# Kernel optimization log

Measured on AMD Instinct MI355X. Metric: run time of the kernel, lower is better.

## Reference

```python
import jax, jax.numpy as jnp
import numpy as np

B, S, E, H = 2, 2048, 1024, 16
D = E // H


def setup_inputs() -> dict:
    key = jax.random.key(0)
    ks = jax.random.split(key, 8)
    hidden_states = jax.random.normal(ks[0], (B, S, E), dtype=jnp.float32)
    # q/k/v projections: small random init
    Wq = jax.random.normal(ks[1], (E, E), dtype=jnp.float32) * 0.02
    Wk = jax.random.normal(ks[2], (E, E), dtype=jnp.float32) * 0.02
    Wv = jax.random.normal(ks[3], (E, E), dtype=jnp.float32) * 0.02
    bq = jnp.zeros((E,), jnp.float32)
    bk = jnp.zeros((E,), jnp.float32)
    bv = jnp.zeros((E,), jnp.float32)
    # hedgehog feature maps: identity init (per init_weights_) + small noise
    eye = jnp.eye(E, dtype=jnp.float32)
    Wfq = eye + jax.random.normal(ks[4], (E, E), dtype=jnp.float32) * 0.02
    Wfk = eye + jax.random.normal(ks[5], (E, E), dtype=jnp.float32) * 0.02
    bfq = jnp.zeros((E,), jnp.float32)
    bfk = jnp.zeros((E,), jnp.float32)
    return dict(hidden_states=hidden_states, Wq=Wq, bq=bq, Wk=Wk, bk=bk,
                Wv=Wv, bv=bv, Wfq=Wfq, bfq=bfq, Wfk=Wfk, bfk=bfk)


def reference(hidden_states, Wq, bq, Wk, bk, Wv, bv, Wfq, bfq, Wfk, bfk):
    b, s, e = hidden_states.shape
    d = e // H
    # feature maps: linear -> linear -> softmax over full hidden dim (before head split)
    q = jax.nn.softmax((hidden_states @ Wq.T + bq) @ Wfq.T + bfq, axis=-1)
    k = jax.nn.softmax((hidden_states @ Wk.T + bk) @ Wfk.T + bfk, axis=-1)
    v = hidden_states @ Wv.T + bv
    split = lambda t: t.reshape(b, s, H, d).transpose(0, 2, 1, 3)  # [B,H,S,D]
    q, k, v = split(q), split(k), split(v)
    scores = jnp.einsum('bhsd,bhtd->bhst', q, k)          # [B,H,S,S], nonnegative
    probs = scores / jnp.sum(scores, axis=-1, keepdims=True)  # sum-normalization
    ctx = jnp.einsum('bhst,bhtd->bhsd', probs, v)
    return ctx.transpose(0, 2, 1, 3).reshape(b, s, e)
```

## Files before the change

kernel.cpp:

```cpp
#include <hip/hip_runtime.h>
#include <math.h>

constexpr int B = 2, S = 2048, E = 1024, H = 16, D = 64;
constexpr int M = B * S;
constexpr int NBIG = 3072;
constexpr int CH = 8;

typedef __attribute__((ext_vector_type(8))) _Float16 half8;
typedef __attribute__((ext_vector_type(4))) float f32x4;
#define MFMA_F16 __builtin_amdgcn_mfma_f32_16x16x32_f16
#define WAITCNT_VM(N) __builtin_amdgcn_s_waitcnt(0xF70 | (N))

__device__ __forceinline__ short f2h(float f) {
  _Float16 h = (_Float16)f;
  short s;
  __builtin_memcpy(&s, &h, 2);
  return s;
}
__device__ __forceinline__ float h2f(short s) {
  _Float16 h;
  __builtin_memcpy(&h, &s, 2);
  return (float)h;
}

__device__ __forceinline__ void gload16(const void* g, const void* l) {
  __builtin_amdgcn_global_load_lds(
      (const __attribute__((address_space(1))) unsigned*)g,
      (__attribute__((address_space(3))) unsigned*)l, 16, 0, 0);
}

template <int BM>
__device__ __forceinline__ void gemm_core(const short* __restrict__ A,
                                          const short* __restrict__ Bm,
                                          int bm, int bn, int K, short* lds,
                                          f32x4 (&acc)[BM / 32][4]) {
  constexpr int SA = BM / 16, TOT = SA + 8, PW = TOT / 4, MT = BM / 32;
  const int tid = threadIdx.x, wave = tid >> 6, lane = tid & 63;

  const short* gb[PW];
#pragma unroll
  for (int j = 0; j < PW; ++j) {
    const int n = wave * PW + j;
    const short* src; int seg, rowbase;
    if (n < SA) { src = A;  seg = n;      rowbase = bm; }
    else        { src = Bm; seg = n - SA; rowbase = bn; }
    const int r = seg * 16 + (lane >> 2);
    const int p = lane & 3;
    const int q = (p - ((r >> 1) & 3)) & 3;
    gb[j] = src + (size_t)(rowbase + r) * K + q * 8;
  }
  const int fr = lane & 15, fq = lane >> 4;
  const int wm = (wave & 1) * (BM / 2), wn = (wave >> 1) * 64;
  int ao[MT], bo[4];
#pragma unroll
  for (int mi = 0; mi < MT; ++mi) {
    const int r = wm + mi * 16 + fr;
    ao[mi] = r * 32 + (((fq + ((r >> 1) & 3)) & 3)) * 8;
  }
#pragma unroll
  for (int ni = 0; ni < 4; ++ni) {
    const int r = wn + ni * 16 + fr;
    bo[ni] = BM * 32 + r * 32 + (((fq + ((r >> 1) & 3)) & 3)) * 8;
  }
  const int ldsW = wave * PW * 512;
  auto stageAll = [&](int buf, int k0) {
#pragma unroll
    for (int j = 0; j < PW; ++j)
      gload16(gb[j] + k0, &lds[buf * TOT * 512 + ldsW + j * 512]);
  };
  stageAll(0, 0);
  stageAll(1, 32);
  int buf = 0;
  for (int k0 = 0; k0 < K; k0 += 32) {
    if (k0 + 32 < K) WAITCNT_VM(PW); else WAITCNT_VM(0);
    __builtin_amdgcn_s_barrier();
    half8 ah[MT], bh4[4];
    const int bb = buf * TOT * 512;
#pragma unroll
    for (int mi = 0; mi < MT; ++mi) ah[mi] = *(const half8*)&lds[bb + ao[mi]];
#pragma unroll
    for (int ni = 0; ni < 4; ++ni) bh4[ni] = *(const half8*)&lds[bb + bo[ni]];
#pragma unroll
    for (int mi = 0; mi < MT; ++mi)
#pragma unroll
      for (int ni = 0; ni < 4; ++ni)
        acc[mi][ni] = MFMA_F16(ah[mi], bh4[ni], acc[mi][ni], 0, 0, 0);
    __builtin_amdgcn_s_barrier();
    if (k0 + 64 < K) stageAll(buf, k0 + 64);
    buf ^= 1;
  }
}

__global__ __launch_bounds__(256) void prep_w(
    const float* __restrict__ Wfq, short* Wfq_f,
    const float* __restrict__ Wfk, short* Wfk_f,
    const float* __restrict__ Wv, short* Wv_f,
    const float* __restrict__ Wq, short* WqT_f,
    const float* __restrict__ Wk, short* WkT_f,
    const float* __restrict__ bq, const float* __restrict__ bfq,
    const float* __restrict__ bk, const float* __restrict__ bfk,
    const float* __restrict__ bv, float* bcat, float* Zk) {
  __shared__ float tb[32][33];
  const int blk = blockIdx.x, tid = threadIdx.x;
  if (blk < 768) {
    const int base = blk;
    const float* src = (base < 256) ? Wfq : (base < 512 ? Wfk : Wv);
    short* dst = (base < 256) ? Wfq_f : (base < 512 ? Wfk_f : Wv_f);
    const int bb = base & 255;
#pragma unroll
    for (int p = 0; p < 4; ++p) {
      const int i = bb * 1024 + p * 256 + tid;
      float4 v = ((const float4*)src)[i];
      ((short4*)dst)[i] = make_short4(f2h(v.x), f2h(v.y), f2h(v.z), f2h(v.w));
    }
  } else if (blk < 2816) {
    const int t = blk - 768;
    const float* in = (t < 1024) ? Wq : Wk;
    short* oh = (t < 1024) ? WqT_f : WkT_f;
    const int tt = t & 1023;
    const int bx = (tt & 31) * 32, by = (tt >> 5) * 32;
    const int x = tid & 31, y0 = tid >> 5;
#pragma unroll
    for (int i = 0; i < 32; i += 8) tb[y0 + i][x] = in[(size_t)(by + y0 + i) * E + bx + x];
    __syncthreads();
#pragma unroll
    for (int i = 0; i < 32; i += 8)
      oh[(size_t)(bx + y0 + i) * E + by + x] = f2h(tb[x][y0 + i]);
  } else if (blk < 3328) {
    const int t = blk - 2816;
    const float* Wf = (t < 256) ? Wfq : Wfk;
    const float* bin = (t < 256) ? bq : bk;
    const float* bf = (t < 256) ? bfq : bfk;
    float* o = (t < 256) ? bcat : bcat + 1024;
    const int n = (t & 255) * 4 + (tid >> 6);
    const int lane = tid & 63;
    float sacc = 0.f;
    for (int j = lane; j < E; j += 64) sacc += Wf[(size_t)n * E + j] * bin[j];
#pragma unroll
    for (int off = 32; off; off >>= 1) sacc += __shfl_xor(sacc, off, 64);
    if (lane == 0) o[n] = sacc + bf[n];
  } else {
    ((float4*)(bcat + 2048))[tid] = ((const float4*)bv)[tid];
#pragma unroll
    for (int p = 0; p < 4; ++p)
      ((float4*)Zk)[p * 256 + tid] = make_float4(0.f, 0.f, 0.f, 0.f);
  }
}

__global__ __launch_bounds__(256, 3) void wgemm_hs(
    const short* __restrict__ Wfq_f, const short* __restrict__ WqT_f,
    const short* __restrict__ Wfk_f, const short* __restrict__ WkT_f,
    short* __restrict__ Wcat,
    const float* __restrict__ hs, short* __restrict__ hs_f) {
  __shared__ short lds[2 * 12 * 512];
  if (blockIdx.z == 2) {
    const int bid = blockIdx.y * 16 + blockIdx.x;
    const int stride = 128 * 256;
    for (int i = bid * 256 + threadIdx.x; i < M * E / 4; i += stride) {
      float4 v = ((const float4*)hs)[i];
      ((short4*)hs_f)[i] = make_short4(f2h(v.x), f2h(v.y), f2h(v.z), f2h(v.w));
    }
    return;
  }
  const short* A = blockIdx.z ? Wfk_f : Wfq_f;
  const short* Bm = blockIdx.z ? WkT_f : WqT_f;
  short* C = Wcat + (size_t)blockIdx.z * E * E;
  const int bm = blockIdx.x * 64, bn = blockIdx.y * 128;
  f32x4 acc[2][4] = {};
  gemm_core<64>(A, Bm, bm, bn, E, lds, acc);
  const int lane = threadIdx.x & 63, wave = threadIdx.x >> 6;
  const int fr = lane & 15, fq = lane >> 4;
  const int wm = (wave & 1) * 32, wn = (wave >> 1) * 64;
#pragma unroll
  for (int ni = 0; ni < 4; ++ni) {
    const int n = bn + wn + ni * 16 + fr;
#pragma unroll
    for (int mi = 0; mi < 2; ++mi) {
      const int m0 = bm + wm + mi * 16 + fq * 4;
#pragma unroll
      for (int r2 = 0; r2 < 4; ++r2)
        C[(size_t)(m0 + r2) * E + n] = f2h(acc[mi][ni][r2]);
    }
  }
}

__global__ __launch_bounds__(256, 3) void gemm_big(
    const short* __restrict__ hs_f, const short* __restrict__ Wcat,
    const float* __restrict__ bcat, short* __restrict__ Cb,
    float* __restrict__ Zk) {
  __shared__ short lds[2 * 16 * 512];
  const int bm = blockIdx.y * 128, bn = blockIdx.x * 128;
  f32x4 acc[4][4] = {};
  gemm_core<128>(hs_f, Wcat, bm, bn, E, lds, acc);
  const int lane = threadIdx.x & 63, wave = threadIdx.x >> 6;
  const int fr = lane & 15, fq = lane >> 4;
  const int wm = (wave & 1) * 64, wn = (wave >> 1) * 64;
  const bool doExp = (bn < 2048);
  const bool doZ = (bn >= 1024) && (bn < 2048);
  float bv4[4];
#pragma unroll
  for (int ni = 0; ni < 4; ++ni) bv4[ni] = bcat[bn + wn + ni * 16 + fr];
#pragma unroll
  for (int mi = 0; mi < 4; ++mi)
#pragma unroll
    for (int r2 = 0; r2 < 4; ++r2) {
      const int m = bm + wm + mi * 16 + fq * 4 + r2;
      float vals[4];
#pragma unroll
      for (int ni = 0; ni < 4; ++ni) vals[ni] = acc[mi][ni][r2] + bv4[ni];
      if (doExp) {
#pragma unroll
        for (int ni = 0; ni < 4; ++ni) vals[ni] = __expf(vals[ni]);
      }
      if (doZ) {
        float es = vals[0] + vals[1] + vals[2] + vals[3];
#pragma unroll
        for (int off = 1; off < 16; off <<= 1) es += __shfl_xor(es, off, 16);
        if (fr == 0) atomicAdd(&Zk[m], es);
      }
#pragma unroll
      for (int ni = 0; ni < 4; ++ni)
        Cb[(size_t)m * NBIG + bn + wn + ni * 16 + fr] = f2h(vals[ni]);
    }
}

__global__ __launch_bounds__(512) void kv_part(const short* __restrict__ Cb,
                                               const float* __restrict__ Zk,
                                               float* __restrict__ KVp,
                                               float* __restrict__ ksump) {
  const int bh = blockIdx.x;
  const int b = bh / H, h = bh % H;
  const int t0 = blockIdx.y * 256;
  const short* kbase = Cb + (size_t)b * S * NBIG + 1024 + h * D;
  const short* vbase = Cb + (size_t)b * S * NBIG + 2048 + h * D;
  __shared__ float ks[32][D];
  __shared__ float vs[32][D];
  __shared__ float invZs[256];
  __shared__ float red[20][256];
  const int tid = threadIdx.x;
  if (tid < 256) invZs[tid] = 1.0f / Zk[b * S + t0 + tid];
  const int t2 = tid & 255;
  const int g = tid >> 8;
  const int a4 = t2 & 15, b4 = t2 >> 4;
  const int lt = tid >> 4, d4 = (tid & 15) * 4;
  float acc[4][4] = {};
  float ksm[4] = {};
  for (int ts = 0; ts < 256; ts += 32) {
    __syncthreads();
    const size_t roff = (size_t)(t0 + ts + lt) * NBIG + d4;
    short4 k4 = *(const short4*)(kbase + roff);
    short4 v4 = *(const short4*)(vbase + roff);
    const float iz = invZs[ts + lt];
    ks[lt][d4 + 0] = h2f(k4.x) * iz; ks[lt][d4 + 1] = h2f(k4.y) * iz;
    ks[lt][d4 + 2] = h2f(k4.z) * iz; ks[lt][d4 + 3] = h2f(k4.w) * iz;
    vs[lt][d4 + 0] = h2f(v4.x); vs[lt][d4 + 1] = h2f(v4.y);
    vs[lt][d4 + 2] = h2f(v4.z); vs[lt][d4 + 3] = h2f(v4.w);
    __syncthreads();
    const int tb = g * 16;
#pragma unroll
    for (int tt = 0; tt < 16; ++tt) {
      float kk4[4], vv4[4];
#pragma unroll
      for (int i = 0; i < 4; ++i) kk4[i] = ks[tb + tt][a4 * 4 + i];
#pragma unroll
      for (int j = 0; j < 4; ++j) vv4[j] = vs[tb + tt][b4 * 4 + j];
#pragma unroll
      for (int i = 0; i < 4; ++i) {
        ksm[i] += kk4[i];
#pragma unroll
        for (int j = 0; j < 4; ++j) acc[i][j] = fmaf(kk4[i], vv4[j], acc[i][j]);
      }
    }
  }
  __syncthreads();
  if (g) {
#pragma unroll
    for (int e = 0; e < 16; ++e) red[e][t2] = acc[e >> 2][e & 3];
#pragma unroll
    for (int i = 0; i < 4; ++i) red[16 + i][t2] = ksm[i];
  }
  __syncthreads();
  if (!g) {
#pragma unroll
    for (int i = 0; i < 4; ++i) {
      ksm[i] += red[16 + i][t2];
#pragma unroll
      for (int j = 0; j < 4; ++j) acc[i][j] += red[i * 4 + j][t2];
    }
    float* kvout = KVp + ((size_t)bh * CH + blockIdx.y) * 4096;
#pragma unroll
    for (int i = 0; i < 4; ++i)
      *(float4*)&kvout[(a4 * 4 + i) * 64 + b4 * 4] =
          make_float4(acc[i][0], acc[i][1], acc[i][2], acc[i][3]);
    if (b4 == 0)
      *(float4*)&ksump[((size_t)bh * CH + blockIdx.y) * 64 + a4 * 4] =
          make_float4(ksm[0], ksm[1], ksm[2], ksm[3]);
  }
}

__global__ __launch_bounds__(256) void out_v8(const short* __restrict__ Cb,
                                              const float* __restrict__ KVp,
                                              const float* __restrict__ ksump,
                                              float* __restrict__ out) {
  const int bh = blockIdx.x;
  const int b = bh >> 4, h = bh & 15;
  __shared__ float KVs[64][64];
  __shared__ float kss[64];
  __shared__ float qs[4][4][64];
  const int tid = threadIdx.x, wave = tid >> 6, lane = tid & 63;
  const int r2 = lane >> 4, g = lane & 15;
  for (int i = tid; i < 1024; i += 256) {
    float4 s = make_float4(0.f, 0.f, 0.f, 0.f);
#pragma unroll
    for (int c = 0; c < CH; ++c) {
      float4 p = ((const float4*)(KVp + ((size_t)bh * CH + c) * 4096))[i];
      s.x += p.x; s.y += p.y; s.z += p.z; s.w += p.w;
    }
    ((float4*)KVs)[i] = s;
  }
  if (tid < 16) {
    float4 s = make_float4(0.f, 0.f, 0.f, 0.f);
#pragma unroll
    for (int c = 0; c < CH; ++c) {
      float4 p = ((const float4*)(ksump + ((size_t)bh * CH + c) * 64))[tid];
      s.x += p.x; s.y += p.y; s.z += p.z; s.w += p.w;
    }
    ((float4*)kss)[tid] = s;
  }
  __syncthreads();
  const float4 ks4 = *(const float4*)&kss[g * 4];
  const int row0 = blockIdx.y * 64 + wave * 16;
#pragma unroll
  for (int it = 0; it < 4; ++it) {
    const int row = row0 + it * 4 + r2;
    short4 us = *(const short4*)(Cb + (size_t)(b * S + row) * NBIG + h * 64 + g * 4);
    float4 u = make_float4(h2f(us.x), h2f(us.y), h2f(us.z), h2f(us.w));
    float dn = u.x * ks4.x + u.y * ks4.y + u.z * ks4.z + u.w * ks4.w;
#pragma unroll
    for (int off = 1; off < 16; off <<= 1) dn += __shfl_xor(dn, off, 16);
    *(float4*)&qs[wave][r2][g * 4] = u;
    __syncthreads();
    float nx = 0.f, ny = 0.f, nz = 0.f, nw = 0.f;
#pragma unroll
    for (int d = 0; d < 64; ++d) {
      const float qd = qs[wave][r2][d];
      const float4 kv = *(const float4*)&KVs[d][g * 4];
      nx = fmaf(qd, kv.x, nx); ny = fmaf(qd, kv.y, ny);
      nz = fmaf(qd, kv.z, nz); nw = fmaf(qd, kv.w, nw);
    }
    const float inv = 1.0f / dn;
    float4 o4 = make_float4(nx * inv, ny * inv, nz * inv, nw * inv);
    const size_t rowoff = ((size_t)b * S + row) * E + h * 64 + g * 4;
    *(float4*)(out + rowoff) = o4;
    __syncthreads();
  }
}

extern "C" void kernel_launch(void* const* d_in, const int* in_sizes, int n_in,
                              void* d_out, int out_size, void* d_ws, size_t ws_size,
                              hipStream_t stream) {
  const float* hs = (const float*)d_in[0];
  const float* Wq = (const float*)d_in[1];
  const float* bq = (const float*)d_in[2];
  const float* Wk = (const float*)d_in[3];
  const float* bk = (const float*)d_in[4];
  const float* Wv = (const float*)d_in[5];
  const float* bv = (const float*)d_in[6];
  const float* Wfq = (const float*)d_in[7];
  const float* bfq = (const float*)d_in[8];
  const float* Wfk = (const float*)d_in[9];
  const float* bfk = (const float*)d_in[10];
  float* out = (float*)d_out;

  const size_t MEG = 1024 * 1024;
  float* ws = (float*)d_ws;
  short* hs_f = (short*)ws;
  short* Wfq_f = (short*)(ws + 2 * MEG);
  short* Wfk_f = (short*)(ws + 2 * MEG + MEG / 2);
  short* WqT_f = (short*)(ws + 3 * MEG);
  short* WkT_f = (short*)(ws + 3 * MEG + MEG / 2);
  short* Wcat = (short*)(ws + 4 * MEG);
  short* Wv_f = Wcat + 2 * MEG;
  float* bcat = ws + 6 * MEG;
  float* Zk = bcat + 4096;
  float* KVp = ws + 7 * MEG;
  float* ksump = ws + 8 * MEG;
  short* Cbig = (short*)(ws + 9 * MEG);

  prep_w<<<3329, 256, 0, stream>>>(Wfq, Wfq_f, Wfk, Wfk_f, Wv, Wv_f,
                                   Wq, WqT_f, Wk, WkT_f,
                                   bq, bfq, bk, bfk, bv, bcat, Zk);
  wgemm_hs<<<dim3(16, 8, 3), 256, 0, stream>>>(Wfq_f, WqT_f, Wfk_f, WkT_f,
                                               Wcat, hs, hs_f);
  gemm_big<<<dim3(24, 32), 256, 0, stream>>>(hs_f, Wcat, bcat, Cbig, Zk);
  kv_part<<<dim3(B * H, CH), 512, 0, stream>>>(Cbig, Zk, KVp, ksump);
  out_v8<<<dim3(B * H, S / 64), 256, 0, stream>>>(Cbig, KVp, ksump, out);
}
```

Before: 180.4 us.

## Enlarge weight-GEMM tiles, vectorize kv LDS reads, register-tile output kernel

Three separate changes. The weight-fusion GEMM now uses 128x128 tiles instead of 64x128, which halves its grid and also shrinks the block count of the fused hs conversion branch. The kv_part inner loop reads LDS as float4 vectors instead of scalars. The output kernel is rewritten to load each Q row once with 16-byte loads, stage Q transposed in LDS, and compute a 4x4 register tile per thread; this removes the per-iteration syncthreads and shuffle reductions. The tradeoff is fewer blocks, hence less parallelism, for the weight GEMM and the conversion work, plus more LDS per block.

```diff
diff --git a/kernel.cpp b/kernel.cpp
--- a/kernel.cpp
+++ b/kernel.cpp
@@ -7,6 +7,7 @@
 constexpr int CH = 8;
 
 typedef __attribute__((ext_vector_type(8))) _Float16 half8;
+typedef __attribute__((ext_vector_type(8))) short short8;
 typedef __attribute__((ext_vector_type(4))) float f32x4;
 #define MFMA_F16 __builtin_amdgcn_mfma_f32_16x16x32_f16
 #define WAITCNT_VM(N) __builtin_amdgcn_s_waitcnt(0xF70 | (N))
@@ -152,10 +153,10 @@
     const short* __restrict__ Wfk_f, const short* __restrict__ WkT_f,
     short* __restrict__ Wcat,
     const float* __restrict__ hs, short* __restrict__ hs_f) {
-  __shared__ short lds[2 * 12 * 512];
+  __shared__ short lds[2 * 16 * 512];
   if (blockIdx.z == 2) {
-    const int bid = blockIdx.y * 16 + blockIdx.x;
-    const int stride = 128 * 256;
+    const int bid = blockIdx.y * 8 + blockIdx.x;
+    const int stride = 64 * 256;
     for (int i = bid * 256 + threadIdx.x; i < M * E / 4; i += stride) {
       float4 v = ((const float4*)hs)[i];
       ((short4*)hs_f)[i] = make_short4(f2h(v.x), f2h(v.y), f2h(v.z), f2h(v.w));
@@ -165,17 +166,17 @@
   const short* A = blockIdx.z ? Wfk_f : Wfq_f;
   const short* Bm = blockIdx.z ? WkT_f : WqT_f;
   short* C = Wcat + (size_t)blockIdx.z * E * E;
-  const int bm = blockIdx.x * 64, bn = blockIdx.y * 128;
-  f32x4 acc[2][4] = {};
-  gemm_core<64>(A, Bm, bm, bn, E, lds, acc);
+  const int bm = blockIdx.x * 128, bn = blockIdx.y * 128;
+  f32x4 acc[4][4] = {};
+  gemm_core<128>(A, Bm, bm, bn, E, lds, acc);
   const int lane = threadIdx.x & 63, wave = threadIdx.x >> 6;
   const int fr = lane & 15, fq = lane >> 4;
-  const int wm = (wave & 1) * 32, wn = (wave >> 1) * 64;
+  const int wm = (wave & 1) * 64, wn = (wave >> 1) * 64;
 #pragma unroll
   for (int ni = 0; ni < 4; ++ni) {
     const int n = bn + wn + ni * 16 + fr;
 #pragma unroll
-    for (int mi = 0; mi < 2; ++mi) {
+    for (int mi = 0; mi < 4; ++mi) {
       const int m0 = bm + wm + mi * 16 + fq * 4;
 #pragma unroll
       for (int r2 = 0; r2 < 4; ++r2)
@@ -259,11 +260,10 @@
     const int tb = g * 16;
 #pragma unroll
     for (int tt = 0; tt < 16; ++tt) {
-      float kk4[4], vv4[4];
-#pragma unroll
-      for (int i = 0; i < 4; ++i) kk4[i] = ks[tb + tt][a4 * 4 + i];
-#pragma unroll
-      for (int j = 0; j < 4; ++j) vv4[j] = vs[tb + tt][b4 * 4 + j];
+      const float4 kk = *(const float4*)&ks[tb + tt][a4 * 4];
+      const float4 vv = *(const float4*)&vs[tb + tt][b4 * 4];
+      const float kk4[4] = {kk.x, kk.y, kk.z, kk.w};
+      const float vv4[4] = {vv.x, vv.y, vv.z, vv.w};
 #pragma unroll
       for (int i = 0; i < 4; ++i) {
         ksm[i] += kk4[i];
@@ -298,7 +298,7 @@
   }
 }
 
-__global__ __launch_bounds__(256) void out_v8(const short* __restrict__ Cb,
+__global__ __launch_bounds__(256) void out_v9(const short* __restrict__ Cb,
                                               const float* __restrict__ KVp,
                                               const float* __restrict__ ksump,
                                               float* __restrict__ out) {
@@ -306,9 +306,16 @@
   const int b = bh >> 4, h = bh & 15;
   __shared__ float KVs[64][64];
   __shared__ float kss[64];
-  __shared__ float qs[4][4][64];
+  __shared__ float qs_t[4][64][20];
+  __shared__ float dns[64];
   const int tid = threadIdx.x, wave = tid >> 6, lane = tid & 63;
-  const int r2 = lane >> 4, g = lane & 15;
+  const int g = lane & 15, rg = lane >> 4;
+  const int row0 = blockIdx.y * 64;
+  const int qrow = row0 + wave * 16 + g;
+  const int dstart = rg * 16;
+  const short* qp = Cb + (size_t)(b * S + qrow) * NBIG + h * 64 + dstart;
+  const short8 u8a = *(const short8*)qp;
+  const short8 u8b = *(const short8*)(qp + 8);
   for (int i = tid; i < 1024; i += 256) {
     float4 s = make_float4(0.f, 0.f, 0.f, 0.f);
 #pragma unroll
@@ -328,31 +335,39 @@
     ((float4*)kss)[tid] = s;
   }
   __syncthreads();
-  const float4 ks4 = *(const float4*)&kss[g * 4];
-  const int row0 = blockIdx.y * 64 + wave * 16;
-#pragma unroll
-  for (int it = 0; it < 4; ++it) {
-    const int row = row0 + it * 4 + r2;
-    short4 us = *(const short4*)(Cb + (size_t)(b * S + row) * NBIG + h * 64 + g * 4);
-    float4 u = make_float4(h2f(us.x), h2f(us.y), h2f(us.z), h2f(us.w));
-    float dn = u.x * ks4.x + u.y * ks4.y + u.z * ks4.z + u.w * ks4.w;
-#pragma unroll
-    for (int off = 1; off < 16; off <<= 1) dn += __shfl_xor(dn, off, 16);
-    *(float4*)&qs[wave][r2][g * 4] = u;
-    __syncthreads();
-    float nx = 0.f, ny = 0.f, nz = 0.f, nw = 0.f;
-#pragma unroll
-    for (int d = 0; d < 64; ++d) {
-      const float qd = qs[wave][r2][d];
-      const float4 kv = *(const float4*)&KVs[d][g * 4];
-      nx = fmaf(qd, kv.x, nx); ny = fmaf(qd, kv.y, ny);
-      nz = fmaf(qd, kv.z, nz); nw = fmaf(qd, kv.w, nw);
-    }
-    const float inv = 1.0f / dn;
-    float4 o4 = make_float4(nx * inv, ny * inv, nz * inv, nw * inv);
-    const size_t rowoff = ((size_t)b * S + row) * E + h * 64 + g * 4;
-    *(float4*)(out + rowoff) = o4;
-    __syncthreads();
+  float uf[16];
+#pragma unroll
+  for (int j = 0; j < 8; ++j) { uf[j] = h2f(u8a[j]); uf[8 + j] = h2f(u8b[j]); }
+  float dnp = 0.f;
+#pragma unroll
+  for (int j = 0; j < 16; ++j) {
+    qs_t[wave][dstart + j][g] = uf[j];
+    dnp = fmaf(uf[j], kss[dstart + j], dnp);
+  }
+  dnp += __shfl_xor(dnp, 16, 64);
+  dnp += __shfl_xor(dnp, 32, 64);
+  if (rg == 0) dns[wave * 16 + g] = dnp;
+  __syncthreads();
+  float acc[4][4] = {};
+#pragma unroll
+  for (int d = 0; d < 64; ++d) {
+    const float4 kv = *(const float4*)&KVs[d][g * 4];
+    const float4 q4 = *(const float4*)&qs_t[wave][d][rg * 4];
+    const float qa[4] = {q4.x, q4.y, q4.z, q4.w};
+    const float ka[4] = {kv.x, kv.y, kv.z, kv.w};
+#pragma unroll
+    for (int i = 0; i < 4; ++i)
+#pragma unroll
+      for (int j = 0; j < 4; ++j) acc[i][j] = fmaf(qa[i], ka[j], acc[i][j]);
+  }
+#pragma unroll
+  for (int i = 0; i < 4; ++i) {
+    const int r = wave * 16 + rg * 4 + i;
+    const float inv = 1.0f / dns[r];
+    const int row = row0 + r;
+    float4 o4 = make_float4(acc[i][0] * inv, acc[i][1] * inv,
+                            acc[i][2] * inv, acc[i][3] * inv);
+    *(float4*)(out + ((size_t)b * S + row) * E + h * 64 + g * 4) = o4;
   }
 }
 
@@ -390,9 +405,9 @@
   prep_w<<<3329, 256, 0, stream>>>(Wfq, Wfq_f, Wfk, Wfk_f, Wv, Wv_f,
                                    Wq, WqT_f, Wk, WkT_f,
                                    bq, bfq, bk, bfk, bv, bcat, Zk);
-  wgemm_hs<<<dim3(16, 8, 3), 256, 0, stream>>>(Wfq_f, WqT_f, Wfk_f, WkT_f,
-                                               Wcat, hs, hs_f);
+  wgemm_hs<<<dim3(8, 8, 3), 256, 0, stream>>>(Wfq_f, WqT_f, Wfk_f, WkT_f,
+                                              Wcat, hs, hs_f);
   gemm_big<<<dim3(24, 32), 256, 0, stream>>>(hs_f, Wcat, bcat, Cbig, Zk);
   kv_part<<<dim3(B * H, CH), 512, 0, stream>>>(Cbig, Zk, KVp, ksump);
-  out_v8<<<dim3(B * H, S / 64), 256, 0, stream>>>(Cbig, KVp, ksump, out);
-}
+  out_v9<<<dim3(B * H, S / 64), 256, 0, stream>>>(Cbig, KVp, ksump, out);
+}
```

Measured after the change: 180.3 us, median of 3. Within noise of the previous version (-0.1%).
